# Optimization experiments

Hardware: AMD Instinct MI355X
Metric: run time of the kernel (lower is better)

## Reference

```python
import jax, jax.numpy as jnp
import numpy as np

LN_EPS = 1e-5


def setup_inputs() -> dict:
    key = jax.random.key(0)
    ks = jax.random.split(key, 6)
    B, M, N, D = 16, 128, 128, 128
    NM, H = 16, 512
    xav = float(np.sqrt(2.0 / (D + D)))  # xavier_normal over (in_dim, out_dim) fan
    return {
        "x": jax.random.normal(ks[0], (B, M, N, D), jnp.float32),
        "w1": jax.random.normal(ks[1], (D, D, NM, 2), jnp.float32) * xav,
        "w2": jax.random.normal(ks[2], (D, D, NM, 2), jnp.float32) * xav,
        "ff_w0": jax.random.normal(ks[3], (D, H), jnp.float32) * float(1.0 / np.sqrt(D)),
        "ff_b0": jnp.zeros((H,), jnp.float32),
        "ff_w1": jax.random.normal(ks[4], (H, D), jnp.float32) * float(1.0 / np.sqrt(H)),
        "ff_b1": jnp.zeros((D,), jnp.float32),
        "ln_g": jnp.ones((D,), jnp.float32),
        "ln_b": jnp.zeros((D,), jnp.float32),
    }


def _layer_norm(h, g, b):
    mu = jnp.mean(h, axis=-1, keepdims=True)
    var = jnp.mean(jnp.square(h - mu), axis=-1, keepdims=True)
    return (h - mu) * jax.lax.rsqrt(var + LN_EPS) * g + b


def _forward_fourier(x, w1, w2):
    # x: [B, M, N, I] -> [B, I, M, N]
    xt = jnp.transpose(x, (0, 3, 1, 2))
    B, I, M, N = xt.shape
    nm = w1.shape[2]
    cw1 = w1[..., 0] + 1j * w1[..., 1]  # [I, O, nm]
    cw2 = w2[..., 0] + 1j * w2[..., 1]
    O = cw1.shape[1]

    # Fourier along last axis (y)
    fty = jnp.fft.rfft(xt, axis=-1, norm="ortho")                    # [B,I,M,N//2+1]
    f1 = jnp.einsum("bixy,ioy->boxy", fty[..., :nm], cw1)            # [B,O,M,nm]
    pad_y = jnp.zeros((B, O, M, N // 2 + 1 - nm), dtype=f1.dtype)
    xy = jnp.fft.irfft(jnp.concatenate([f1, pad_y], axis=-1), n=N, axis=-1, norm="ortho")

    # Fourier along second-to-last axis (x)
    ftx = jnp.fft.rfft(xt, axis=-2, norm="ortho")                    # [B,I,M//2+1,N]
    f2 = jnp.einsum("bixy,iox->boxy", ftx[:, :, :nm, :], cw2)        # [B,O,nm,N]
    pad_x = jnp.zeros((B, O, M // 2 + 1 - nm, N), dtype=f2.dtype)
    xx = jnp.fft.irfft(jnp.concatenate([f2, pad_x], axis=-2), n=M, axis=-2, norm="ortho")

    return jnp.transpose(xx + xy, (0, 2, 3, 1))  # [B,M,N,O]


def reference(x, w1, w2, ff_w0, ff_b0, ff_w1, ff_b1, ln_g, ln_b):
    h = _forward_fourier(x, w1, w2)
    # backcast FeedForward: Linear -> ReLU -> Linear -> LayerNorm (dropout=0)
    h1 = jax.nn.relu(jnp.einsum("bmni,ih->bmnh", h, ff_w0) + ff_b0)
    h2 = jnp.einsum("bmnh,ho->bmno", h1, ff_w1) + ff_b1
    return _layer_norm(h2, ln_g, ln_b)
```

## Files before the change

### kernel.cpp

```cpp
#include <hip/hip_runtime.h>


#define LN_EPS 1e-5f
#define NMODES 16
#define FROW 4096
#define HROW 16384

typedef __attribute__((ext_vector_type(8))) short short8;
typedef __attribute__((ext_vector_type(8))) ushort ushort8;
typedef __attribute__((ext_vector_type(4))) short short4v;
typedef __attribute__((ext_vector_type(4))) float f32x4;

__device__ __forceinline__ ushort f2bf(float f) {
    unsigned u = __float_as_uint(f);
    unsigned r = (u + 0x7FFFu + ((u >> 16) & 1u)) >> 16;
    return (ushort)r;
}
__device__ __forceinline__ float bf2f(ushort h) {
    return __uint_as_float(((unsigned)h) << 16);
}

__global__ void k_setup(float* __restrict__ Tc, float* __restrict__ Ts,
                        float* __restrict__ IT) {
    const float invs = 0.08838834764831845f;
    for (int idx = threadIdx.x; idx < NMODES * 128; idx += blockDim.x) {
        int k = idx >> 7, n = idx & 127;
        int p = (k * n) & 127;
        float th = (float)p * (6.283185307179586f / 128.0f);
        float c = cosf(th), s = sinf(th);
        Tc[idx] = c * invs;
        Ts[idx] = -s * invs;
        float ck = (k == 0) ? invs : 2.0f * invs;
        IT[n * 32 + 2 * k]     = ck * c;
        IT[n * 32 + 2 * k + 1] = -ck * s;
    }
}

__global__ void k_wpack(const float* __restrict__ w, ushort* __restrict__ Wph,
                        ushort* __restrict__ Wpl) {
    int idx = blockIdx.x * 256 + threadIdx.x;
    int k  = idx >> 16;
    int op = (idx >> 8) & 255;
    int ip = idx & 255;
    int i = ip & 127, o = op & 127;
    const float* base = w + (((i << 7) | o) * NMODES + k) * 2;
    float re = base[0], im = base[1];
    float v = (ip < 128) ? ((op < 128) ? re : im)
                         : ((op < 128) ? -im : re);
    ushort hi = f2bf(v);
    ushort lo = f2bf(v - bf2f(hi));
    Wph[idx] = hi;
    Wpl[idx] = lo;
}

__global__ __launch_bounds__(256) void k_wcvt(const float* __restrict__ w0,
        const float* __restrict__ w1, ushort* __restrict__ w0t,
        ushort* __restrict__ w1t) {
    int idx = blockIdx.x * 256 + threadIdx.x;
    int h = idx >> 7, k = idx & 127;
    w0t[idx] = f2bf(w0[k * 512 + h]);
    int o = idx >> 9, hh = idx & 511;
    w1t[idx] = f2bf(w1[hh * 128 + o]);
}

__global__ __launch_bounds__(128) void k_fft(const float* __restrict__ x,
        const float* __restrict__ Tc, const float* __restrict__ Ts,
        float* __restrict__ F, int mode) {
    __shared__ float Tc_s[NMODES * 128];
    __shared__ float Ts_s[NMODES * 128];
    for (int e = threadIdx.x; e < NMODES * 128; e += 128) {
        Tc_s[e] = Tc[e];
        Ts_s[e] = Ts[e];
    }
    __syncthreads();
    int row = blockIdx.x;
    int base, ts;
    if (mode == 0) { base = row * HROW; ts = 128; }
    else { base = (row >> 7) * 2097152 + (row & 127) * 128; ts = 16384; }
    int i = threadIdx.x;
    float re[NMODES], im[NMODES];
#pragma unroll
    for (int k = 0; k < NMODES; ++k) { re[k] = 0.f; im[k] = 0.f; }
    for (int tb = 0; tb < 32; ++tb) {
        int t0 = tb * 4;
        float xv0 = x[base + (t0 + 0) * ts + i];
        float xv1 = x[base + (t0 + 1) * ts + i];
        float xv2 = x[base + (t0 + 2) * ts + i];
        float xv3 = x[base + (t0 + 3) * ts + i];
#pragma unroll
        for (int k = 0; k < NMODES; ++k) {
            f32x4 c4 = *(const f32x4*)&Tc_s[k * 128 + t0];
            f32x4 s4 = *(const f32x4*)&Ts_s[k * 128 + t0];
            re[k] += xv0 * c4[0] + xv1 * c4[1] + xv2 * c4[2] + xv3 * c4[3];
            im[k] += xv0 * s4[0] + xv1 * s4[1] + xv2 * s4[2] + xv3 * s4[3];
        }
    }
    float* outp = F + row * FROW;
#pragma unroll
    for (int k = 0; k < NMODES; ++k) {
        outp[k * 256 + i]       = re[k];
        outp[k * 256 + 128 + i] = im[k];
    }
}

__global__ __launch_bounds__(256) void k_mixm(const float* __restrict__ A,
        const ushort* __restrict__ Wph, const ushort* __restrict__ Wpl,
        float* __restrict__ outF) {
    __shared__ ushort Ah[32 * 264];
    __shared__ ushort Al[32 * 264];
    int tid = threadIdx.x;
    int kt = blockIdx.x & 15;
    int bm0 = (blockIdx.x >> 4) * 32;
    {
        int row = tid >> 3, cg = tid & 7;
        const float* arow = A + (bm0 + row) * FROW + kt * 256 + cg * 32;
        ushort* ah = &Ah[row * 264 + cg * 32];
        ushort* al = &Al[row * 264 + cg * 32];
#pragma unroll
        for (int j = 0; j < 8; ++j) {
            f32x4 v = *(const f32x4*)(arow + j * 4);
            short4v h4, l4;
#pragma unroll
            for (int q = 0; q < 4; ++q) {
                ushort h = f2bf(v[q]);
                h4[q] = (short)h;
                l4[q] = (short)f2bf(v[q] - bf2f(h));
            }
            *(short4v*)(ah + j * 4) = h4;
            *(short4v*)(al + j * 4) = l4;
        }
    }
    __syncthreads();
    int lane = tid & 63, wid = tid >> 6;
    int frow = lane & 15, fk8 = (lane >> 4) * 8, fr4 = (lane >> 4) * 4;
    f32x4 acc[2][4];
#pragma unroll
    for (int a = 0; a < 2; ++a)
#pragma unroll
        for (int c = 0; c < 4; ++c) acc[a][c] = {0.f, 0.f, 0.f, 0.f};
    const ushort* wph = Wph + kt * 65536;
    const ushort* wpl = Wpl + kt * 65536;
#pragma unroll
    for (int kk = 0; kk < 8; ++kk) {
        short8 ah0 = *(const short8*)&Ah[(frow)      * 264 + kk * 32 + fk8];
        short8 ah1 = *(const short8*)&Ah[(16 + frow) * 264 + kk * 32 + fk8];
        short8 al0 = *(const short8*)&Al[(frow)      * 264 + kk * 32 + fk8];
        short8 al1 = *(const short8*)&Al[(16 + frow) * 264 + kk * 32 + fk8];
#pragma unroll
        for (int tc = 0; tc < 4; ++tc) {
            int op = wid * 64 + tc * 16 + frow;
            int base = op * 256 + kk * 32 + fk8;
            short8 wh = *(const short8*)&wph[base];
            short8 wl = *(const short8*)&wpl[base];
            acc[0][tc] = __builtin_amdgcn_mfma_f32_16x16x32_bf16(ah0, wh, acc[0][tc], 0, 0, 0);
            acc[0][tc] = __builtin_amdgcn_mfma_f32_16x16x32_bf16(ah0, wl, acc[0][tc], 0, 0, 0);
            acc[0][tc] = __builtin_amdgcn_mfma_f32_16x16x32_bf16(al0, wh, acc[0][tc], 0, 0, 0);
            acc[1][tc] = __builtin_amdgcn_mfma_f32_16x16x32_bf16(ah1, wh, acc[1][tc], 0, 0, 0);
            acc[1][tc] = __builtin_amdgcn_mfma_f32_16x16x32_bf16(ah1, wl, acc[1][tc], 0, 0, 0);
            acc[1][tc] = __builtin_amdgcn_mfma_f32_16x16x32_bf16(al1, wh, acc[1][tc], 0, 0, 0);
        }
    }
#pragma unroll
    for (int tr = 0; tr < 2; ++tr)
#pragma unroll
        for (int tc = 0; tc < 4; ++tc)
#pragma unroll
            for (int r = 0; r < 4; ++r)
                outF[(bm0 + tr * 16 + fr4 + r) * FROW + kt * 256 + wid * 64 + tc * 16 + frow]
                    = acc[tr][tc][r];
}

__global__ __launch_bounds__(256) void k_icdft(const float* __restrict__ f,
        const float* __restrict__ IT, ushort* __restrict__ obf,
        float* __restrict__ h32, const ushort* __restrict__ hyin, int mode) {
    __shared__ float IT_s[128 * 32];
    __shared__ float f_s[32 * 128];
    int row = blockIdx.x;
    for (int e = threadIdx.x; e < 4096; e += 256) {
        IT_s[e] = IT[e];
        f_s[e]  = f[row * FROW + e];
    }
    __syncthreads();
    int o = threadIdx.x & 127, nh = threadIdx.x >> 7;
    for (int nb = 0; nb < 8; ++nb) {
        int n0 = nh * 64 + nb * 8;
        float acc[8];
#pragma unroll
        for (int j = 0; j < 8; ++j) acc[j] = 0.f;
#pragma unroll
        for (int kpb = 0; kpb < 8; ++kpb) {
            int kp0 = kpb * 4;
            float f0 = f_s[kp0 * 128 + o];
            float f1v = f_s[kp0 * 128 + 128 + o];
            float f2v = f_s[kp0 * 128 + 256 + o];
            float f3v = f_s[kp0 * 128 + 384 + o];
#pragma unroll
            for (int j = 0; j < 8; ++j) {
                f32x4 it = *(const f32x4*)&IT_s[(n0 + j) * 32 + kp0];
                acc[j] += f0 * it[0] + f1v * it[1] + f2v * it[2] + f3v * it[3];
            }
        }
        if (mode == 0) {
#pragma unroll
            for (int j = 0; j < 8; ++j)
                obf[row * HROW + (n0 + j) * 128 + o] = f2bf(acc[j]);
        } else if (mode == 1) {
#pragma unroll
            for (int j = 0; j < 8; ++j)
                h32[row * HROW + (n0 + j) * 128 + o] = acc[j];
        } else if (mode == 2) {
#pragma unroll
            for (int j = 0; j < 8; ++j) {
                int ix = (row >> 7) * 2097152 + (row & 127) * 128 + o + (n0 + j) * 16384;
                obf[ix] = f2bf(bf2f(hyin[ix]) + acc[j]);
            }
        } else {
#pragma unroll
            for (int j = 0; j < 8; ++j) {
                int ix = (row >> 7) * 2097152 + (row & 127) * 128 + o + (n0 + j) * 16384;
                obf[ix] = f2bf(h32[ix] + acc[j]);
            }
        }
    }
}

__global__ __launch_bounds__(128, 3) void k_ffn(const ushort* __restrict__ hin,
        float* __restrict__ out,
        const ushort* __restrict__ w0t, const float* __restrict__ b0,
        const ushort* __restrict__ w1t, const float* __restrict__ b1,
        const float* __restrict__ g, const float* __restrict__ bb) {
    __shared__ __align__(16) char h_raw[16384];
    __shared__ __align__(16) char h1_raw[2][5120];
    __shared__ float ps_s[128];
    __shared__ float pq_s[128];
    int tid = threadIdx.x;
    int wave = tid >> 6, lane = tid & 63;
    int R0 = blockIdx.x * 64;

    {
        const ushort* src = hin + (size_t)R0 * 128;
#pragma unroll
        for (int i = 0; i < 8; ++i) {
            int e = tid + i * 128;
            int rl = e >> 4, c8 = e & 15;
            ushort8 v = *(const ushort8*)(src + rl * 128 + c8 * 8);
            *(ushort8*)(h_raw + rl * 256 + ((c8 ^ (rl & 7)) << 4)) = v;
        }
    }
    __syncthreads();

    int frow = lane & 15, qg = lane >> 4;
    int fk8 = qg * 8, fr4 = qg * 4;
    int sw7 = frow & 7;

    f32x4 acc2[4][4];
#pragma unroll
    for (int a = 0; a < 4; ++a)
#pragma unroll
        for (int c = 0; c < 4; ++c) acc2[a][c] = {0.f, 0.f, 0.f, 0.f};

    short8 bfr[4];
#pragma unroll
    for (int kk = 0; kk < 4; ++kk)
        bfr[kk] = *(const short8*)&w0t[(wave * 16 + frow) * 128 + kk * 32 + fk8];

#pragma unroll 1
    for (int ch = 0; ch < 16; ++ch) {
        short8 b2[4];
#pragma unroll
        for (int tc = 0; tc < 4; ++tc)
            b2[tc] = *(const short8*)&w1t[(wave * 64 + tc * 16 + frow) * 512 + ch * 32 + fk8];
        float b0v = b0[ch * 32 + wave * 16 + frow];

        f32x4 acc1[4];
#pragma unroll
        for (int a = 0; a < 4; ++a) acc1[a] = {0.f, 0.f, 0.f, 0.f};
#pragma unroll
        for (int kk = 0; kk < 4; ++kk)
#pragma unroll
            for (int tr = 0; tr < 4; ++tr) {
                short8 av = *(const short8*)(h_raw + (tr * 16 + frow) * 256
                             + (((kk * 4 + qg) ^ sw7) << 4));
                acc1[tr] = __builtin_amdgcn_mfma_f32_16x16x32_bf16(
                    av, bfr[kk], acc1[tr], 0, 0, 0);
            }
        char* h1w = h1_raw[ch & 1];
#pragma unroll
        for (int tr = 0; tr < 4; ++tr)
#pragma unroll
            for (int r = 0; r < 4; ++r)
                *(ushort*)(h1w + (tr * 16 + fr4 + r) * 80 + wave * 32 + frow * 2) =
                    f2bf(fmaxf(acc1[tr][r] + b0v, 0.f));

        if (ch < 15) {
#pragma unroll
            for (int kk = 0; kk < 4; ++kk)
                bfr[kk] = *(const short8*)
                    &w0t[((ch + 1) * 32 + wave * 16 + frow) * 128 + kk * 32 + fk8];
        }

        asm volatile("s_waitcnt lgkmcnt(0)" ::: "memory");
        __builtin_amdgcn_s_barrier();
        asm volatile("" ::: "memory");

#pragma unroll
        for (int tr = 0; tr < 4; ++tr) {
            short8 a2 = *(const short8*)(h1w + (tr * 16 + frow) * 80 + qg * 16);
#pragma unroll
            for (int tc = 0; tc < 4; ++tc)
                acc2[tr][tc] = __builtin_amdgcn_mfma_f32_16x16x32_bf16(
                    a2, b2[tc], acc2[tr][tc], 0, 0, 0);
        }
    }

    float b1v[4], gv[4], bv[4];
#pragma unroll
    for (int tc = 0; tc < 4; ++tc) {
        int o = wave * 64 + tc * 16 + frow;
        b1v[tc] = b1[o]; gv[tc] = g[o]; bv[tc] = bb[o];
    }
#pragma unroll
    for (int tr = 0; tr < 4; ++tr)
#pragma unroll
        for (int r = 0; r < 4; ++r) {
            float s = 0.f, qq = 0.f;
#pragma unroll
            for (int tc = 0; tc < 4; ++tc) {
                float v = acc2[tr][tc][r] + b1v[tc];
                acc2[tr][tc][r] = v;
                s += v; qq += v * v;
            }
            s += __shfl_xor(s, 1); qq += __shfl_xor(qq, 1);
            s += __shfl_xor(s, 2); qq += __shfl_xor(qq, 2);
            s += __shfl_xor(s, 4); qq += __shfl_xor(qq, 4);
            s += __shfl_xor(s, 8); qq += __shfl_xor(qq, 8);
            if (frow == 0) {
                int row = tr * 16 + fr4 + r;
                ps_s[wave * 64 + row] = s;
                pq_s[wave * 64 + row] = qq;
            }
        }
    __syncthreads();
#pragma unroll
    for (int tr = 0; tr < 4; ++tr)
#pragma unroll
        for (int r = 0; r < 4; ++r) {
            int row = tr * 16 + fr4 + r;
            float S = ps_s[row] + ps_s[64 + row];
            float Q = pq_s[row] + pq_s[64 + row];
            float mu = S * (1.0f / 128.0f);
            float var = Q * (1.0f / 128.0f) - mu * mu;
            float rs = rsqrtf(fmaxf(var, 0.f) + LN_EPS);
            float* orow = &out[(size_t)(R0 + row) * 128 + wave * 64];
#pragma unroll
            for (int tc = 0; tc < 4; ++tc)
                orow[tc * 16 + frow] = (acc2[tr][tc][r] - mu) * rs * gv[tc] + bv[tc];
        }
}

extern "C" void kernel_launch(void* const* d_in, const int* in_sizes, int n_in,
                              void* d_out, int out_size, void* d_ws, size_t ws_size,
                              hipStream_t stream) {
    (void)in_sizes; (void)n_in; (void)out_size;
    const float* x   = (const float*)d_in[0];
    const float* w1  = (const float*)d_in[1];
    const float* w2  = (const float*)d_in[2];
    const float* fw0 = (const float*)d_in[3];
    const float* fb0 = (const float*)d_in[4];
    const float* fw1 = (const float*)d_in[5];
    const float* fb1 = (const float*)d_in[6];
    const float* lng = (const float*)d_in[7];
    const float* lnb = (const float*)d_in[8];
    float* out = (float*)d_out;

    char* ws = (char*)d_ws;
    float*  Tc  = (float*)(ws);
    float*  Ts  = (float*)(ws + 8192);
    float*  IT  = (float*)(ws + 16384);
    ushort* Wph = (ushort*)(ws + 32768);
    ushort* Wpl = (ushort*)(ws + 32768 + 2097152);
    ushort* w0t = (ushort*)(ws + 4227072);
    ushort* w1t = (ushort*)(ws + 4358144);
    float*  buf0 = (float*)(ws + 4489216);
    ushort* hy   = (ushort*)(ws + 38043648);
    ushort* hsum = (ushort*)(ws + 105152512);
    const size_t need_two = 172261376ull;
    int two = (ws_size >= need_two) ? 1 : 0;
    ushort* hbfs = hy;

    k_setup<<<1, 256, 0, stream>>>(Tc, Ts, IT);
    k_wcvt <<<256, 256, 0, stream>>>(fw0, fw1, w0t, w1t);

    k_wpack<<<4096, 256, 0, stream>>>(w1, Wph, Wpl);
    k_fft  <<<2048, 128, 0, stream>>>(x, Tc, Ts, buf0, 0);
    k_mixm <<<1024, 256, 0, stream>>>(buf0, Wph, Wpl, buf0);
    if (two) k_icdft<<<2048, 256, 0, stream>>>(buf0, IT, hy, out, hy, 0);
    else     k_icdft<<<2048, 256, 0, stream>>>(buf0, IT, hy, out, hy, 1);

    k_wpack<<<4096, 256, 0, stream>>>(w2, Wph, Wpl);
    k_fft  <<<2048, 128, 0, stream>>>(x, Tc, Ts, buf0, 1);
    k_mixm <<<1024, 256, 0, stream>>>(buf0, Wph, Wpl, buf0);
    if (two) k_icdft<<<2048, 256, 0, stream>>>(buf0, IT, hsum, out, hy, 2);
    else     k_icdft<<<2048, 256, 0, stream>>>(buf0, IT, hbfs, out, hy, 3);

    k_ffn<<<4096, 128, 0, stream>>>(two ? hsum : hbfs, out,
                                    w0t, fb0, w1t, fb1, lng, lnb);
}
```

Before: 492.5 us.

## Split fused FFN into two GEMM kernels with bf16 hidden buffer in chunks

Replaces the single fused FFN kernel, which recomputed the hidden layer per 64-row tile with per-chunk barriers, with two separate GEMM kernels. The first writes the ReLU hidden activations to a bf16 workspace and the second runs the 512-wide reduction plus bias and LayerNorm. Rows are processed in chunks so the intermediate fits in existing scratch buffers, and the second kernel uses a simple register-prefetch double step. This adds a global memory round trip for the 512-wide hidden tensor and more launches, in exchange for larger, more regular GEMM tiles and higher occupancy.

Result: slower. 567.4 us (+15.2%).

```diff
diff --git a/kernel.cpp b/kernel.cpp
--- a/kernel.cpp
+++ b/kernel.cpp
@@ -224,110 +224,157 @@
     }
 }
 
-__global__ __launch_bounds__(128, 3) void k_ffn(const ushort* __restrict__ hin,
-        float* __restrict__ out,
+__global__ __launch_bounds__(256) void k_ffn1(const ushort* __restrict__ hin,
         const ushort* __restrict__ w0t, const float* __restrict__ b0,
+        ushort* __restrict__ h1o) {
+    __shared__ ushort A_l[128 * 136];
+    __shared__ ushort B_l[64 * 136];
+    int tid = threadIdx.x;
+    int ht = blockIdx.x & 7, rt = blockIdx.x >> 3;
+    int R0 = rt * 128, H0 = ht * 64;
+
+#pragma unroll
+    for (int i = 0; i < 8; ++i) {
+        int e = tid + i * 256;
+        int row = e >> 4, c16 = e & 15;
+        *(ushort8*)&A_l[row * 136 + c16 * 8] =
+            *(const ushort8*)(hin + (size_t)(R0 + row) * 128 + c16 * 8);
+    }
+#pragma unroll
+    for (int i = 0; i < 4; ++i) {
+        int e = tid + i * 256;
+        int row = e >> 4, c16 = e & 15;
+        *(ushort8*)&B_l[row * 136 + c16 * 8] =
+            *(const ushort8*)(w0t + (H0 + row) * 128 + c16 * 8);
+    }
+    __syncthreads();
+
+    int lane = tid & 63, wave = tid >> 6;
+    int frow = lane & 15, qg = lane >> 4, fk8 = qg * 8, fr4 = qg * 4;
+    int r2 = wave >> 1, c2 = wave & 1;
+
+    f32x4 acc[4][2];
+#pragma unroll
+    for (int a = 0; a < 4; ++a)
+#pragma unroll
+        for (int c = 0; c < 2; ++c) acc[a][c] = {0.f, 0.f, 0.f, 0.f};
+
+#pragma unroll
+    for (int kk = 0; kk < 4; ++kk) {
+        short8 af[4], bf[2];
+#pragma unroll
+        for (int tr = 0; tr < 4; ++tr)
+            af[tr] = *(const short8*)&A_l[(r2 * 64 + tr * 16 + frow) * 136 + kk * 32 + fk8];
+#pragma unroll
+        for (int tc = 0; tc < 2; ++tc)
+            bf[tc] = *(const short8*)&B_l[(c2 * 32 + tc * 16 + frow) * 136 + kk * 32 + fk8];
+#pragma unroll
+        for (int tr = 0; tr < 4; ++tr)
+#pragma unroll
+            for (int tc = 0; tc < 2; ++tc)
+                acc[tr][tc] = __builtin_amdgcn_mfma_f32_16x16x32_bf16(
+                    af[tr], bf[tc], acc[tr][tc], 0, 0, 0);
+    }
+
+    float b0v[2];
+    b0v[0] = b0[H0 + c2 * 32 + frow];
+    b0v[1] = b0[H0 + c2 * 32 + 16 + frow];
+#pragma unroll
+    for (int tr = 0; tr < 4; ++tr)
+#pragma unroll
+        for (int tc = 0; tc < 2; ++tc)
+#pragma unroll
+            for (int r = 0; r < 4; ++r) {
+                int row = r2 * 64 + tr * 16 + fr4 + r;
+                int col = H0 + c2 * 32 + tc * 16 + frow;
+                h1o[(size_t)(R0 + row) * 512 + col] =
+                    f2bf(fmaxf(acc[tr][tc][r] + b0v[tc], 0.f));
+            }
+}
+
+__global__ __launch_bounds__(256) void k_ffn2(const ushort* __restrict__ h1,
         const ushort* __restrict__ w1t, const float* __restrict__ b1,
-        const float* __restrict__ g, const float* __restrict__ bb) {
-    __shared__ __align__(16) char h_raw[16384];
-    __shared__ __align__(16) char h1_raw[2][5120];
+        const float* __restrict__ g, const float* __restrict__ bb,
+        float* __restrict__ out) {
+    __shared__ ushort A_l[32 * 72];
+    __shared__ ushort B_l[128 * 72];
     __shared__ float ps_s[128];
     __shared__ float pq_s[128];
     int tid = threadIdx.x;
-    int wave = tid >> 6, lane = tid & 63;
-    int R0 = blockIdx.x * 64;
-
-    {
-        const ushort* src = hin + (size_t)R0 * 128;
-#pragma unroll
-        for (int i = 0; i < 8; ++i) {
-            int e = tid + i * 128;
-            int rl = e >> 4, c8 = e & 15;
-            ushort8 v = *(const ushort8*)(src + rl * 128 + c8 * 8);
-            *(ushort8*)(h_raw + rl * 256 + ((c8 ^ (rl & 7)) << 4)) = v;
-        }
-    }
-    __syncthreads();
-
-    int frow = lane & 15, qg = lane >> 4;
-    int fk8 = qg * 8, fr4 = qg * 4;
-    int sw7 = frow & 7;
-
-    f32x4 acc2[4][4];
-#pragma unroll
-    for (int a = 0; a < 4; ++a)
-#pragma unroll
-        for (int c = 0; c < 4; ++c) acc2[a][c] = {0.f, 0.f, 0.f, 0.f};
-
-    short8 bfr[4];
-#pragma unroll
-    for (int kk = 0; kk < 4; ++kk)
-        bfr[kk] = *(const short8*)&w0t[(wave * 16 + frow) * 128 + kk * 32 + fk8];
+    int R0 = blockIdx.x * 32;
+    int lane = tid & 63, wave = tid >> 6;
+    int frow = lane & 15, qg = lane >> 4, fk8 = qg * 8, fr4 = qg * 4;
+    int sAr = tid >> 3, sc8 = tid & 7;
+
+    *(ushort8*)&A_l[sAr * 72 + sc8 * 8] =
+        *(const ushort8*)(h1 + (size_t)(R0 + sAr) * 512 + sc8 * 8);
+#pragma unroll
+    for (int i = 0; i < 4; ++i) {
+        int ro = sAr + i * 32;
+        *(ushort8*)&B_l[ro * 72 + sc8 * 8] =
+            *(const ushort8*)(w1t + ro * 512 + sc8 * 8);
+    }
+    __syncthreads();
+
+    f32x4 acc[2][2];
+#pragma unroll
+    for (int a = 0; a < 2; ++a)
+#pragma unroll
+        for (int c = 0; c < 2; ++c) acc[a][c] = {0.f, 0.f, 0.f, 0.f};
 
 #pragma unroll 1
-    for (int ch = 0; ch < 16; ++ch) {
-        short8 b2[4];
-#pragma unroll
-        for (int tc = 0; tc < 4; ++tc)
-            b2[tc] = *(const short8*)&w1t[(wave * 64 + tc * 16 + frow) * 512 + ch * 32 + fk8];
-        float b0v = b0[ch * 32 + wave * 16 + frow];
-
-        f32x4 acc1[4];
-#pragma unroll
-        for (int a = 0; a < 4; ++a) acc1[a] = {0.f, 0.f, 0.f, 0.f};
-#pragma unroll
-        for (int kk = 0; kk < 4; ++kk)
-#pragma unroll
-            for (int tr = 0; tr < 4; ++tr) {
-                short8 av = *(const short8*)(h_raw + (tr * 16 + frow) * 256
-                             + (((kk * 4 + qg) ^ sw7) << 4));
-                acc1[tr] = __builtin_amdgcn_mfma_f32_16x16x32_bf16(
-                    av, bfr[kk], acc1[tr], 0, 0, 0);
-            }
-        char* h1w = h1_raw[ch & 1];
-#pragma unroll
-        for (int tr = 0; tr < 4; ++tr)
-#pragma unroll
-            for (int r = 0; r < 4; ++r)
-                *(ushort*)(h1w + (tr * 16 + fr4 + r) * 80 + wave * 32 + frow * 2) =
-                    f2bf(fmaxf(acc1[tr][r] + b0v, 0.f));
-
-        if (ch < 15) {
-#pragma unroll
-            for (int kk = 0; kk < 4; ++kk)
-                bfr[kk] = *(const short8*)
-                    &w0t[((ch + 1) * 32 + wave * 16 + frow) * 128 + kk * 32 + fk8];
-        }
-
-        asm volatile("s_waitcnt lgkmcnt(0)" ::: "memory");
-        __builtin_amdgcn_s_barrier();
-        asm volatile("" ::: "memory");
-
-#pragma unroll
-        for (int tr = 0; tr < 4; ++tr) {
-            short8 a2 = *(const short8*)(h1w + (tr * 16 + frow) * 80 + qg * 16);
-#pragma unroll
-            for (int tc = 0; tc < 4; ++tc)
-                acc2[tr][tc] = __builtin_amdgcn_mfma_f32_16x16x32_bf16(
-                    a2, b2[tc], acc2[tr][tc], 0, 0, 0);
-        }
-    }
-
-    float b1v[4], gv[4], bv[4];
-#pragma unroll
-    for (int tc = 0; tc < 4; ++tc) {
-        int o = wave * 64 + tc * 16 + frow;
+    for (int kt = 0; kt < 8; ++kt) {
+        ushort8 sa, sb0, sb1, sb2, sb3;
+        if (kt < 7) {
+            int koff = (kt + 1) * 64 + sc8 * 8;
+            sa  = *(const ushort8*)(h1 + (size_t)(R0 + sAr) * 512 + koff);
+            sb0 = *(const ushort8*)(w1t + (sAr +  0) * 512 + koff);
+            sb1 = *(const ushort8*)(w1t + (sAr + 32) * 512 + koff);
+            sb2 = *(const ushort8*)(w1t + (sAr + 64) * 512 + koff);
+            sb3 = *(const ushort8*)(w1t + (sAr + 96) * 512 + koff);
+        }
+#pragma unroll
+        for (int kk = 0; kk < 2; ++kk) {
+            short8 af[2], bf[2];
+#pragma unroll
+            for (int tr = 0; tr < 2; ++tr)
+                af[tr] = *(const short8*)&A_l[(tr * 16 + frow) * 72 + kk * 32 + fk8];
+#pragma unroll
+            for (int tc = 0; tc < 2; ++tc)
+                bf[tc] = *(const short8*)&B_l[(wave * 32 + tc * 16 + frow) * 72 + kk * 32 + fk8];
+#pragma unroll
+            for (int tr = 0; tr < 2; ++tr)
+#pragma unroll
+                for (int tc = 0; tc < 2; ++tc)
+                    acc[tr][tc] = __builtin_amdgcn_mfma_f32_16x16x32_bf16(
+                        af[tr], bf[tc], acc[tr][tc], 0, 0, 0);
+        }
+        __syncthreads();
+        if (kt < 7) {
+            *(ushort8*)&A_l[sAr * 72 + sc8 * 8] = sa;
+            *(ushort8*)&B_l[(sAr +  0) * 72 + sc8 * 8] = sb0;
+            *(ushort8*)&B_l[(sAr + 32) * 72 + sc8 * 8] = sb1;
+            *(ushort8*)&B_l[(sAr + 64) * 72 + sc8 * 8] = sb2;
+            *(ushort8*)&B_l[(sAr + 96) * 72 + sc8 * 8] = sb3;
+            __syncthreads();
+        }
+    }
+
+    float b1v[2], gv[2], bv[2];
+#pragma unroll
+    for (int tc = 0; tc < 2; ++tc) {
+        int o = wave * 32 + tc * 16 + frow;
         b1v[tc] = b1[o]; gv[tc] = g[o]; bv[tc] = bb[o];
     }
 #pragma unroll
-    for (int tr = 0; tr < 4; ++tr)
+    for (int tr = 0; tr < 2; ++tr)
 #pragma unroll
         for (int r = 0; r < 4; ++r) {
             float s = 0.f, qq = 0.f;
 #pragma unroll
-            for (int tc = 0; tc < 4; ++tc) {
-                float v = acc2[tr][tc][r] + b1v[tc];
-                acc2[tr][tc][r] = v;
+            for (int tc = 0; tc < 2; ++tc) {
+                float v = acc[tr][tc][r] + b1v[tc];
+                acc[tr][tc][r] = v;
                 s += v; qq += v * v;
             }
             s += __shfl_xor(s, 1); qq += __shfl_xor(qq, 1);
@@ -336,25 +383,24 @@
             s += __shfl_xor(s, 8); qq += __shfl_xor(qq, 8);
             if (frow == 0) {
                 int row = tr * 16 + fr4 + r;
-                ps_s[wave * 64 + row] = s;
-                pq_s[wave * 64 + row] = qq;
-            }
-        }
-    __syncthreads();
-#pragma unroll
-    for (int tr = 0; tr < 4; ++tr)
+                ps_s[wave * 32 + row] = s;
+                pq_s[wave * 32 + row] = qq;
+            }
+        }
+    __syncthreads();
+#pragma unroll
+    for (int tr = 0; tr < 2; ++tr)
 #pragma unroll
         for (int r = 0; r < 4; ++r) {
             int row = tr * 16 + fr4 + r;
-            float S = ps_s[row] + ps_s[64 + row];
-            float Q = pq_s[row] + pq_s[64 + row];
+            float S = ps_s[row] + ps_s[32 + row] + ps_s[64 + row] + ps_s[96 + row];
+            float Q = pq_s[row] + pq_s[32 + row] + pq_s[64 + row] + pq_s[96 + row];
             float mu = S * (1.0f / 128.0f);
             float var = Q * (1.0f / 128.0f) - mu * mu;
             float rs = rsqrtf(fmaxf(var, 0.f) + LN_EPS);
-            float* orow = &out[(size_t)(R0 + row) * 128 + wave * 64];
-#pragma unroll
-            for (int tc = 0; tc < 4; ++tc)
-                orow[tc * 16 + frow] = (acc2[tr][tc][r] - mu) * rs * gv[tc] + bv[tc];
+            float* orow = &out[(size_t)(R0 + row) * 128 + wave * 32];
+            orow[frow]      = (acc[tr][0][r] - mu) * rs * gv[0] + bv[0];
+            orow[16 + frow] = (acc[tr][1][r] - mu) * rs * gv[1] + bv[1];
         }
 }
 
@@ -403,6 +449,18 @@
     if (two) k_icdft<<<2048, 256, 0, stream>>>(buf0, IT, hsum, out, hy, 2);
     else     k_icdft<<<2048, 256, 0, stream>>>(buf0, IT, hbfs, out, hy, 3);
 
-    k_ffn<<<4096, 128, 0, stream>>>(two ? hsum : hbfs, out,
-                                    w0t, fb0, w1t, fb1, lng, lnb);
-}
+    if (two) {
+        for (int c = 0; c < 4; ++c) {
+            const size_t off = (size_t)c * 65536 * 128;
+            k_ffn1<<<4096, 256, 0, stream>>>(hsum + off, w0t, fb0, hy);
+            k_ffn2<<<2048, 256, 0, stream>>>(hy, w1t, fb1, lng, lnb, out + off);
+        }
+    } else {
+        ushort* h1buf = (ushort*)buf0;
+        for (int c = 0; c < 8; ++c) {
+            const size_t off = (size_t)c * 32768 * 128;
+            k_ffn1<<<2048, 256, 0, stream>>>(hbfs + off, w0t, fb0, h1buf);
+            k_ffn2<<<1024, 256, 0, stream>>>(h1buf, w1t, fb1, lng, lnb, out + off);
+        }
+    }
+}
```
